# Performance work log

Measured on AMD Instinct MI355X. Metric: run time of the kernel, lower is better.

The kernel has to match this reference:

```python
import jax, jax.numpy as jnp
import numpy as np

S, B, H = 2048, 2, 4096
NH, NG, HD = 32, 2, 128        # query heads, kv groups, head dim
ROT = 64                        # rotary dims (half of head dim)


def apply_rope(x, rope):
    # x: [s, b, n, hd]; rope: [s, 1, rot//2, 2]
    s = x.shape[0]
    rot = rope.shape[-2] * 2
    xr, xp = x[..., :rot], x[..., rot:]
    xs = xr.reshape(xr.shape[:-1] + (rot // 2, 2))          # [s,b,n,rot/2,2]
    rc = rope[:s].reshape(s, 1, 1, rot // 2, 2)             # broadcast over b, n
    c, sn = rc[..., 0], rc[..., 1]
    x0, x1 = xs[..., 0], xs[..., 1]
    out = jnp.stack([x0 * c - x1 * sn, x1 * c + x0 * sn], axis=-1)
    return jnp.concatenate([out.reshape(xr.shape), xp], axis=-1)


def setup_inputs() -> dict:
    key = jax.random.key(0)
    k1, k2, k3, k4 = jax.random.split(key, 4)
    hidden_states = jax.random.normal(k1, (S, B, H), dtype=jnp.float32)
    # causal boolean mask: True = attend
    causal = jnp.tril(jnp.ones((S, S), dtype=bool))
    attention_mask = jnp.broadcast_to(causal[None, None], (B, 1, S, S))
    # standard RoPE cache: [s, 1, rot//2, 2] = (cos, sin)
    pos = jnp.arange(S, dtype=jnp.float32)
    inv_freq = 1.0 / (10000.0 ** (jnp.arange(0, ROT // 2, dtype=jnp.float32) / (ROT // 2)))
    ang = pos[:, None] * inv_freq[None, :]
    rotary_pos_emb = jnp.stack([jnp.cos(ang), jnp.sin(ang)], axis=-1)[:, None]
    W_qkv = jax.random.normal(k2, (NH * HD + 2 * NG * HD, H), dtype=jnp.float32) * (H ** -0.5)
    b_qkv = jax.random.normal(k3, (NH * HD + 2 * NG * HD,), dtype=jnp.float32) * 0.02
    W_dense = jax.random.normal(k4, (H, NH * HD), dtype=jnp.float32) * ((NH * HD) ** -0.5)
    return {"hidden_states": hidden_states, "attention_mask": attention_mask,
            "rotary_pos_emb": rotary_pos_emb, "W_qkv": W_qkv, "b_qkv": b_qkv,
            "W_dense": W_dense}


def reference(hidden_states, attention_mask, rotary_pos_emb, W_qkv, b_qkv, W_dense):
    s, b, _ = hidden_states.shape
    r = NH // NG  # query heads per kv group
    mixed = jnp.einsum('sbh,oh->sbo', hidden_states, W_qkv) + b_qkv
    q = mixed[..., :NH * HD].reshape(s, b, NH, HD)
    k = mixed[..., NH * HD:NH * HD + NG * HD].reshape(s, b, NG, HD)
    v = mixed[..., NH * HD + NG * HD:].reshape(s, b, NG, HD)
    q = apply_rope(q, rotary_pos_emb)
    k = apply_rope(k, rotary_pos_emb)
    # GQA: keep kv at NG heads, give q a [g, r] split instead of materializing repeats
    qg = q.reshape(s, b, NG, r, HD)
    scale = HD ** -0.5
    scores = jnp.einsum('sbgrd,tbgd->bgrst', qg, k) * scale     # [b,g,r,s,t]
    mask = attention_mask[:, :, None]                            # [b,1,1,s,t]
    scores = jnp.where(mask, scores, jnp.finfo(scores.dtype).min)
    probs = jax.nn.softmax(scores, axis=-1)
    ctx = jnp.einsum('bgrst,tbgd->sbgrd', probs, v)              # [s,b,g,r,d]
    ctx = ctx.reshape(s, b, NH * HD)
    out = jnp.einsum('sbp,hp->sbh', ctx, W_dense)
    return out
```

## Files before the change

kernel.cpp:

```cpp
#include <hip/hip_runtime.h>
#include <cstdint>
#include <cstddef>


#define S_LEN 2048
#define BATCH 2
#define NHEADS 32
#define NGROUPS 2
#define HEADDIM 128
#define OQKV 4608
#define KSTRIDE 160
#define VSTRIDE 2080

typedef __attribute__((ext_vector_type(4))) float f32x4;
typedef __attribute__((ext_vector_type(4))) unsigned int u32x4;
typedef __attribute__((ext_vector_type(8))) unsigned short u16x8;
typedef __attribute__((ext_vector_type(8))) short s16x8;

union B8 { u32x4 q; u16x8 u; s16x8 s; };

__device__ __forceinline__ unsigned short f2b(float f) {
  unsigned int u = __builtin_bit_cast(unsigned int, f);
  u += 0x7fffu + ((u >> 16) & 1u);
  return (unsigned short)(u >> 16);
}
__device__ __forceinline__ float b2f(unsigned short h) {
  unsigned int u = ((unsigned int)h) << 16;
  return __builtin_bit_cast(float, u);
}

__global__ __launch_bounds__(256) void cvt_kernel(const float* __restrict__ in,
                                                  unsigned short* __restrict__ out) {
  size_t i = (size_t)blockIdx.x * 256 + threadIdx.x;
  const f32x4* p = (const f32x4*)(in + i * 8);
  f32x4 a = p[0], b = p[1];
  B8 r;
  r.u[0] = f2b(a[0]); r.u[1] = f2b(a[1]); r.u[2] = f2b(a[2]); r.u[3] = f2b(a[3]);
  r.u[4] = f2b(b[0]); r.u[5] = f2b(b[1]); r.u[6] = f2b(b[2]); r.u[7] = f2b(b[3]);
  *(u32x4*)(out + i * 8) = r.q;
}

template<int A_FP32, int HAS_BIAS, int OUT_BF16>
__global__ __launch_bounds__(256) void gemm_bt(const void* __restrict__ Ap,
                                               const unsigned short* __restrict__ Bt,
                                               const float* __restrict__ bias,
                                               void* __restrict__ Cp,
                                               int M, int N, int K) {
  __shared__ __align__(16) unsigned short lA[128 * 40];
  __shared__ __align__(16) unsigned short lB[128 * 40];
  const int tid = threadIdx.x;
  const int wave = tid >> 6, lane = tid & 63;
  const int quad = lane >> 4, l15 = lane & 15;
  const int m0 = blockIdx.y * 128, n0 = blockIdx.x * 128;
  const int wm = (wave & 1) * 64, wn = (wave >> 1) * 64;
  const int sr = tid >> 2, sc = (tid & 3) * 8;
  f32x4 acc[4][4] = {};
  const unsigned short* Ab = (const unsigned short*)Ap;
  const float* Af = (const float*)Ap;
  for (int k0 = 0; k0 < K; k0 += 32) {
    B8 a0, a1;
    u32x4 b0, b1;
    if (A_FP32) {
      const f32x4* p0 = (const f32x4*)(Af + (size_t)(m0 + sr) * K + k0 + sc);
      const f32x4* p1 = (const f32x4*)(Af + (size_t)(m0 + sr + 64) * K + k0 + sc);
      f32x4 x0 = p0[0], x1 = p0[1], y0 = p1[0], y1 = p1[1];
      for (int e = 0; e < 4; ++e) {
        a0.u[e] = f2b(x0[e]); a0.u[e + 4] = f2b(x1[e]);
        a1.u[e] = f2b(y0[e]); a1.u[e + 4] = f2b(y1[e]);
      }
    } else {
      a0.q = *(const u32x4*)(Ab + (size_t)(m0 + sr) * K + k0 + sc);
      a1.q = *(const u32x4*)(Ab + (size_t)(m0 + sr + 64) * K + k0 + sc);
    }
    b0 = *(const u32x4*)(Bt + (size_t)(n0 + sr) * K + k0 + sc);
    b1 = *(const u32x4*)(Bt + (size_t)(n0 + sr + 64) * K + k0 + sc);
    __syncthreads();
    *(u32x4*)(lA + sr * 40 + sc) = a0.q;
    *(u32x4*)(lA + (sr + 64) * 40 + sc) = a1.q;
    *(u32x4*)(lB + sr * 40 + sc) = b0;
    *(u32x4*)(lB + (sr + 64) * 40 + sc) = b1;
    __syncthreads();
    B8 af[4], bf[4];
    for (int i = 0; i < 4; ++i)
      af[i].q = *(const u32x4*)(lA + (wm + 16 * i + l15) * 40 + quad * 8);
    for (int j = 0; j < 4; ++j)
      bf[j].q = *(const u32x4*)(lB + (wn + 16 * j + l15) * 40 + quad * 8);
    for (int i = 0; i < 4; ++i)
      for (int j = 0; j < 4; ++j)
        acc[i][j] = __builtin_amdgcn_mfma_f32_16x16x32_bf16(af[i].s, bf[j].s, acc[i][j], 0, 0, 0);
  }
  for (int i = 0; i < 4; ++i) {
    int gm = m0 + wm + 16 * i + quad * 4;
    for (int j = 0; j < 4; ++j) {
      int gn = n0 + wn + 16 * j + l15;
      float bb = HAS_BIAS ? bias[gn] : 0.0f;
      for (int r = 0; r < 4; ++r) {
        float v = acc[i][j][r] + bb;
        if (OUT_BF16)
          ((unsigned short*)Cp)[(size_t)(gm + r) * N + gn] = f2b(v);
        else
          ((float*)Cp)[(size_t)(gm + r) * N + gn] = v;
      }
    }
  }
}

__global__ __launch_bounds__(256) void rope_scatter(const unsigned short* __restrict__ mixed,
                                                    const float* __restrict__ rope,
                                                    unsigned short* __restrict__ qb,
                                                    unsigned short* __restrict__ kb,
                                                    unsigned short* __restrict__ vt) {
  unsigned int idx = blockIdx.x * 256 + threadIdx.x;
  unsigned int row = idx / 2304;
  unsigned int pr = idx - row * 2304;
  unsigned int o = pr * 2;
  unsigned int s = row >> 1, b = row & 1;
  unsigned int pq = *(const unsigned int*)(mixed + (size_t)row * OQKV + o);
  float x0 = b2f((unsigned short)(pq & 0xffff));
  float x1 = b2f((unsigned short)(pq >> 16));
  if (o >= 4352) {
    unsigned int g = (o - 4352) >> 7;
    unsigned int d = (o - 4352) & 127;
    unsigned short* base = vt + ((size_t)(b * NGROUPS + g) * HEADDIM + d) * VSTRIDE + s;
    base[0] = f2b(x0);
    base[VSTRIDE] = f2b(x1);
    return;
  }
  unsigned short* dst;
  unsigned int d;
  bool is_q = (o < 4096);
  if (is_q) {
    unsigned int h = o >> 7; d = o & 127;
    dst = qb + (((size_t)(b * NHEADS + h) * S_LEN + s) * HEADDIM + d);
  } else {
    unsigned int g = (o - 4096) >> 7; d = (o - 4096) & 127;
    dst = kb + (((size_t)(b * NGROUPS + g) * S_LEN + s) * KSTRIDE + d);
  }
  if (d < 64) {
    unsigned int i = d >> 1;
    float c = rope[s * 64 + i * 2], sn = rope[s * 64 + i * 2 + 1];
    float y0 = x0 * c - x1 * sn;
    float y1 = x1 * c + x0 * sn;
    x0 = y0; x1 = y1;
  }
  if (is_q) {
    const float scale = 0.08838834764831845f;
    x0 *= scale; x1 *= scale;
  }
  dst[0] = f2b(x0);
  dst[1] = f2b(x1);
}

__global__ __launch_bounds__(256) void attn_kernel(const unsigned short* __restrict__ qb,
                                                   const unsigned short* __restrict__ kb,
                                                   const unsigned short* __restrict__ vt,
                                                   unsigned short* __restrict__ ctx) {
  __shared__ __align__(16) unsigned short lk[64 * 128];
  __shared__ __align__(16) unsigned short lv[128 * 64];
  __shared__ __align__(16) unsigned short lp[4][16 * 72];
  const int qt = 31 - blockIdx.x;
  const int h = blockIdx.y, b = blockIdx.z;
  const int g = h >> 4;
  const int tid = threadIdx.x;
  const int wave = tid >> 6, lane = tid & 63;
  const int quad = lane >> 4, l15 = lane & 15;
  const int q0 = qt * 64 + wave * 16;
  unsigned short* lpw = lp[wave];
  char* lkb = (char*)lk;
  char* lvb = (char*)lv;

  const unsigned short* qp =
      qb + ((size_t)(b * NHEADS + h) * S_LEN + q0 + l15) * HEADDIM + quad * 8;
  B8 aq[4];
  for (int c = 0; c < 4; ++c) aq[c].q = *(const u32x4*)(qp + 32 * c);

  const unsigned short* kbase = kb + (size_t)(b * NGROUPS + g) * S_LEN * KSTRIDE;
  const unsigned short* vbase = vt + (size_t)(b * NGROUPS + g) * HEADDIM * VSTRIDE;

  const int krow = tid >> 2, kcol = (tid & 3) * 32;
  const int vrow = tid >> 1, vcol = (tid & 1) * 32;
  const int kxs = (krow & 7) << 4, vxs = (vrow & 7) << 4;
  const int kwb = krow * 256 + kcol * 2;
  const int vwb = vrow * 128 + vcol * 2;

  f32x4 o[8] = {};
  float lrow[4] = {0.f, 0.f, 0.f, 0.f};

  B8 kR0, kR1, kR2, kR3, vR0, vR1, vR2, vR3;
  {
    const unsigned short* kg = kbase + (size_t)krow * KSTRIDE + kcol;
    const unsigned short* vg = vbase + (size_t)vrow * VSTRIDE + vcol;
    kR0.q = *(const u32x4*)(kg);      kR1.q = *(const u32x4*)(kg + 8);
    kR2.q = *(const u32x4*)(kg + 16); kR3.q = *(const u32x4*)(kg + 24);
    vR0.q = *(const u32x4*)(vg);      vR1.q = *(const u32x4*)(vg + 8);
    vR2.q = *(const u32x4*)(vg + 16); vR3.q = *(const u32x4*)(vg + 24);
  }

  for (int kt = 0; kt <= qt; ++kt) {
    const int k0 = kt * 64;
    __syncthreads();
    *(u32x4*)(lkb + ((kwb +  0) ^ kxs)) = kR0.q;
    *(u32x4*)(lkb + ((kwb + 16) ^ kxs)) = kR1.q;
    *(u32x4*)(lkb + ((kwb + 32) ^ kxs)) = kR2.q;
    *(u32x4*)(lkb + ((kwb + 48) ^ kxs)) = kR3.q;
    *(u32x4*)(lvb + ((vwb +  0) ^ vxs)) = vR0.q;
    *(u32x4*)(lvb + ((vwb + 16) ^ vxs)) = vR1.q;
    *(u32x4*)(lvb + ((vwb + 32) ^ vxs)) = vR2.q;
    *(u32x4*)(lvb + ((vwb + 48) ^ vxs)) = vR3.q;
    __syncthreads();
    if (kt < qt) {
      const int k1 = k0 + 64;
      const unsigned short* kg = kbase + (size_t)(k1 + krow) * KSTRIDE + kcol;
      const unsigned short* vg = vbase + (size_t)vrow * VSTRIDE + k1 + vcol;
      kR0.q = *(const u32x4*)(kg);      kR1.q = *(const u32x4*)(kg + 8);
      kR2.q = *(const u32x4*)(kg + 16); kR3.q = *(const u32x4*)(kg + 24);
      vR0.q = *(const u32x4*)(vg);      vR1.q = *(const u32x4*)(vg + 8);
      vR2.q = *(const u32x4*)(vg + 16); vR3.q = *(const u32x4*)(vg + 24);
    }
    f32x4 sfr[4] = {};
    for (int t = 0; t < 4; ++t) {
      const int row = 16 * t + l15;
      const int rxs = (row & 7) << 4;
      const int rb = row * 256 + quad * 16;
      for (int c = 0; c < 4; ++c) {
        B8 bk;
        bk.q = *(const u32x4*)(lkb + ((rb + 64 * c) ^ rxs));
        sfr[t] = __builtin_amdgcn_mfma_f32_16x16x32_bf16(aq[c].s, bk.s, sfr[t], 0, 0, 0);
      }
    }
    const bool masked = (kt == qt);
    for (int r = 0; r < 4; ++r) {
      const int qq = q0 + quad * 4 + r;
      float psum = 0.f;
      for (int t = 0; t < 4; ++t) {
        float p = __expf(sfr[t][r]);
        if (masked && (k0 + 16 * t + l15 > qq)) p = 0.f;
        psum += p;
        lpw[(quad * 4 + r) * 72 + 16 * t + l15] = f2b(p);
      }
      lrow[r] += psum;
    }
    B8 pa0, pa1;
    pa0.q = *(const u32x4*)(lpw + l15 * 72 + quad * 8);
    pa1.q = *(const u32x4*)(lpw + l15 * 72 + 32 + quad * 8);
    for (int j = 0; j < 8; ++j) {
      const int row = 16 * j + l15;
      const int rxs = (row & 7) << 4;
      const int rb = row * 128 + quad * 16;
      B8 b0, b1;
      b0.q = *(const u32x4*)(lvb + (rb ^ rxs));
      b1.q = *(const u32x4*)(lvb + ((rb + 64) ^ rxs));
      o[j] = __builtin_amdgcn_mfma_f32_16x16x32_bf16(pa0.s, b0.s, o[j], 0, 0, 0);
      o[j] = __builtin_amdgcn_mfma_f32_16x16x32_bf16(pa1.s, b1.s, o[j], 0, 0, 0);
    }
  }
  float inv[4];
  for (int r = 0; r < 4; ++r) {
    float l = lrow[r];
    l += __shfl_xor(l, 1);
    l += __shfl_xor(l, 2);
    l += __shfl_xor(l, 4);
    l += __shfl_xor(l, 8);
    inv[r] = 1.0f / l;
  }
  for (int j = 0; j < 8; ++j) {
    for (int r = 0; r < 4; ++r) {
      int s = q0 + quad * 4 + r;
      ctx[(size_t)(s * BATCH + b) * 4096 + (size_t)h * HEADDIM + 16 * j + l15] =
          f2b(o[j][r] * inv[r]);
    }
  }
}

extern "C" void kernel_launch(void* const* d_in, const int* in_sizes, int n_in,
                              void* d_out, int out_size, void* d_ws, size_t ws_size,
                              hipStream_t stream) {
  const float* hidden = (const float*)d_in[0];
  const float* rope = (const float*)d_in[2];
  const float* Wqkv = (const float*)d_in[3];
  const float* bqkv = (const float*)d_in[4];
  const float* Wdense = (const float*)d_in[5];
  float* out = (float*)d_out;
  char* ws = (char*)d_ws;

  unsigned short* Wqkv_b   = (unsigned short*)(ws);
  unsigned short* Wdense_b = (unsigned short*)(ws + 37748736);
  unsigned short* mixedb   = (unsigned short*)(ws + 71303168);
  unsigned short* vtbuf    = (unsigned short*)(ws + 109051904);
  unsigned short* qbuf     = (unsigned short*)(ws);
  unsigned short* kbuf     = (unsigned short*)(ws + 33554432);
  unsigned short* ctxb     = (unsigned short*)(ws + 71303168);

  cvt_kernel<<<9216, 256, 0, stream>>>(Wqkv, Wqkv_b);
  cvt_kernel<<<8192, 256, 0, stream>>>(Wdense, Wdense_b);

  gemm_bt<1, 1, 1><<<dim3(36, 32), 256, 0, stream>>>(hidden, Wqkv_b, bqkv, mixedb,
                                                     4096, 4608, 4096);
  rope_scatter<<<36864, 256, 0, stream>>>(mixedb, rope, qbuf, kbuf, vtbuf);
  attn_kernel<<<dim3(32, 32, 2), 256, 0, stream>>>(qbuf, kbuf, vtbuf, ctxb);
  gemm_bt<0, 0, 0><<<dim3(32, 32), 256, 0, stream>>>(ctxb, Wdense_b, nullptr, out,
                                                     4096, 4096, 4096);
}
```

Baseline: 966.9 us.

## Load GEMM tiles directly to LDS and swizzle workgroup order

```diff
diff --git a/kernel.cpp b/kernel.cpp
--- a/kernel.cpp
+++ b/kernel.cpp
@@ -27,6 +27,12 @@
 __device__ __forceinline__ float b2f(unsigned short h) {
   unsigned int u = ((unsigned int)h) << 16;
   return __builtin_bit_cast(float, u);
+}
+
+__device__ __forceinline__ void gload16(const unsigned short* g, unsigned short* l) {
+  __builtin_amdgcn_global_load_lds(
+      (const __attribute__((address_space(1))) void*)g,
+      (__attribute__((address_space(3))) void*)l, 16, 0, 0);
 }
 
 __global__ __launch_bounds__(256) void cvt_kernel(const float* __restrict__ in,
@@ -46,45 +52,56 @@
                                                const float* __restrict__ bias,
                                                void* __restrict__ Cp,
                                                int M, int N, int K) {
-  __shared__ __align__(16) unsigned short lA[128 * 40];
-  __shared__ __align__(16) unsigned short lB[128 * 40];
+  __shared__ __align__(16) unsigned short lA[128 * 32];
+  __shared__ __align__(16) unsigned short lB[128 * 32];
   const int tid = threadIdx.x;
   const int wave = tid >> 6, lane = tid & 63;
   const int quad = lane >> 4, l15 = lane & 15;
-  const int m0 = blockIdx.y * 128, n0 = blockIdx.x * 128;
+  const int nwg = gridDim.x * gridDim.y;
+  int lin = blockIdx.y * gridDim.x + blockIdx.x;
+  int swz = (lin & 7) * (nwg >> 3) + (lin >> 3);
+  const int bx = swz % gridDim.x, by = swz / gridDim.x;
+  const int m0 = by * 128, n0 = bx * 128;
   const int wm = (wave & 1) * 64, wn = (wave >> 1) * 64;
-  const int sr = tid >> 2, sc = (tid & 3) * 8;
+  const int grow = wave * 16 + (lane >> 2);
+  const int gcol = (lane & 3) * 8;
+  unsigned short* lAw = lA + wave * 512;
+  unsigned short* lBw = lB + wave * 512;
   f32x4 acc[4][4] = {};
   const unsigned short* Ab = (const unsigned short*)Ap;
   const float* Af = (const float*)Ap;
+  const int ar = tid >> 1, acf = (tid & 1) * 16;
+  f32x4 x0, x1, x2, x3;
+  if (A_FP32) {
+    const f32x4* p = (const f32x4*)(Af + (size_t)(m0 + ar) * K + acf);
+    x0 = p[0]; x1 = p[1]; x2 = p[2]; x3 = p[3];
+  }
   for (int k0 = 0; k0 < K; k0 += 32) {
-    B8 a0, a1;
-    u32x4 b0, b1;
+    __syncthreads();
     if (A_FP32) {
-      const f32x4* p0 = (const f32x4*)(Af + (size_t)(m0 + sr) * K + k0 + sc);
-      const f32x4* p1 = (const f32x4*)(Af + (size_t)(m0 + sr + 64) * K + k0 + sc);
-      f32x4 x0 = p0[0], x1 = p0[1], y0 = p1[0], y1 = p1[1];
+      B8 c0, c1;
       for (int e = 0; e < 4; ++e) {
-        a0.u[e] = f2b(x0[e]); a0.u[e + 4] = f2b(x1[e]);
-        a1.u[e] = f2b(y0[e]); a1.u[e + 4] = f2b(y1[e]);
+        c0.u[e] = f2b(x0[e]); c0.u[e + 4] = f2b(x1[e]);
+        c1.u[e] = f2b(x2[e]); c1.u[e + 4] = f2b(x3[e]);
       }
+      *(u32x4*)(lA + ar * 32 + acf) = c0.q;
+      *(u32x4*)(lA + ar * 32 + acf + 8) = c1.q;
     } else {
-      a0.q = *(const u32x4*)(Ab + (size_t)(m0 + sr) * K + k0 + sc);
-      a1.q = *(const u32x4*)(Ab + (size_t)(m0 + sr + 64) * K + k0 + sc);
-    }
-    b0 = *(const u32x4*)(Bt + (size_t)(n0 + sr) * K + k0 + sc);
-    b1 = *(const u32x4*)(Bt + (size_t)(n0 + sr + 64) * K + k0 + sc);
+      gload16(Ab + (size_t)(m0 + grow) * K + k0 + gcol, lAw);
+      gload16(Ab + (size_t)(m0 + 64 + grow) * K + k0 + gcol, lAw + 2048);
+    }
+    gload16(Bt + (size_t)(n0 + grow) * K + k0 + gcol, lBw);
+    gload16(Bt + (size_t)(n0 + 64 + grow) * K + k0 + gcol, lBw + 2048);
     __syncthreads();
-    *(u32x4*)(lA + sr * 40 + sc) = a0.q;
-    *(u32x4*)(lA + (sr + 64) * 40 + sc) = a1.q;
-    *(u32x4*)(lB + sr * 40 + sc) = b0;
-    *(u32x4*)(lB + (sr + 64) * 40 + sc) = b1;
-    __syncthreads();
+    if (A_FP32 && k0 + 32 < K) {
+      const f32x4* p = (const f32x4*)(Af + (size_t)(m0 + ar) * K + k0 + 32 + acf);
+      x0 = p[0]; x1 = p[1]; x2 = p[2]; x3 = p[3];
+    }
     B8 af[4], bf[4];
     for (int i = 0; i < 4; ++i)
-      af[i].q = *(const u32x4*)(lA + (wm + 16 * i + l15) * 40 + quad * 8);
+      af[i].q = *(const u32x4*)(lA + (wm + 16 * i + l15) * 32 + quad * 8);
     for (int j = 0; j < 4; ++j)
-      bf[j].q = *(const u32x4*)(lB + (wn + 16 * j + l15) * 40 + quad * 8);
+      bf[j].q = *(const u32x4*)(lB + (wn + 16 * j + l15) * 32 + quad * 8);
     for (int i = 0; i < 4; ++i)
       for (int j = 0; j < 4; ++j)
         acc[i][j] = __builtin_amdgcn_mfma_f32_16x16x32_bf16(af[i].s, bf[j].s, acc[i][j], 0, 0, 0);
```

New measurement: 989.8 us. +2.4%, slower.
